# Kernel optimization log

Measured on AMD Instinct MI355X. Metric: run time of the kernel, lower is better.

Reference implementation:

```python
import jax, jax.numpy as jnp
import numpy as np

THRESHOLD = 0.5  # args.threshold: mask prob >= threshold means 'read' this token
HIDDEN = 256
EMBED = 300
BATCH = 64
STEPS = 2048


def setup_inputs() -> dict:
    key = jax.random.key(0)
    ks = jax.random.split(key, 10)
    H, E = HIDDEN, EMBED
    s = 1.0 / np.sqrt(H)
    return {
        "embedded": jax.random.normal(ks[0], (BATCH, STEPS, E), dtype=jnp.float32),
        "mask": jax.random.uniform(ks[1], (BATCH, STEPS), dtype=jnp.float32),
        "lengths": jax.random.randint(ks[2], (BATCH,), 1, STEPS + 1),
        # LSTM cell params (torch gate order i, f, g, o)
        "W_ih": jax.random.uniform(ks[3], (4 * H, E), minval=-s, maxval=s, dtype=jnp.float32),
        "W_hh": jax.random.uniform(ks[4], (4 * H, H), minval=-s, maxval=s, dtype=jnp.float32),
        "b_ih": jax.random.uniform(ks[5], (4 * H,), minval=-s, maxval=s, dtype=jnp.float32),
        "b_hh": jax.random.uniform(ks[6], (4 * H,), minval=-s, maxval=s, dtype=jnp.float32),
        "W_out": jax.random.uniform(ks[7], (2, H), minval=-s, maxval=s, dtype=jnp.float32),
        "b_out": jax.random.uniform(ks[8], (2,), minval=-s, maxval=s, dtype=jnp.float32),
    }


def reference(embedded, mask, lengths, W_ih, W_hh, b_ih, b_hh, W_out, b_out):
    B, T, E = embedded.shape
    H = W_hh.shape[1]
    b = b_ih + b_hh

    def step(carry, xs):
        h, c = carry
        x_t, m_t = xs  # [B,E], [B]
        z = x_t @ W_ih.T + h @ W_hh.T + b  # [B,4H]
        i, f, g, o = jnp.split(z, 4, axis=-1)
        i = jax.nn.sigmoid(i)
        f = jax.nn.sigmoid(f)
        g = jnp.tanh(g)
        o = jax.nn.sigmoid(o)
        c_new = f * c + i * g
        h_new = o * jnp.tanh(c_new)
        read = (m_t >= THRESHOLD)[:, None]  # skip-RNN gate
        h2 = jnp.where(read, h_new, h)
        c2 = jnp.where(read, c_new, c)
        return (h2, c2), h2

    h0 = jnp.zeros((B, H), embedded.dtype)
    c0 = jnp.zeros((B, H), embedded.dtype)
    xs = (jnp.swapaxes(embedded, 0, 1), mask.T)  # time-major
    _, hs = jax.lax.scan(step, (h0, c0), xs)  # hs: [T,B,H]

    idx = jnp.clip(lengths - 1, 0, T - 1)
    last = hs[idx, jnp.arange(B)]  # [B,H] last relevant output
    logits = last @ W_out.T + b_out
    probs = jax.nn.softmax(logits, axis=-1)
    predictions = jnp.argmax(probs, axis=1)
    return probs, predictions
```

## Files before the change

### kernel.cpp

```cpp
#include <hip/hip_runtime.h>
#include <math.h>

#define BATCH  64
#define TSTEPS 2048
#define EMBED  300
#define HID    256
#define GATES  1024
#define WSTRIDE 36
#define ASTR   328

typedef __fp16 h2 __attribute__((ext_vector_type(2)));
typedef __fp16 h4 __attribute__((ext_vector_type(4)));
typedef __fp16 h8 __attribute__((ext_vector_type(8)));
typedef float  f4 __attribute__((ext_vector_type(4)));

__device__ __forceinline__ h2 pack_h2(float a, float b) {
    return __builtin_amdgcn_cvt_pkrtz(a, b);
}
__device__ __forceinline__ h2 bc_h2(unsigned u) {
    return __builtin_bit_cast(h2, u);
}
__device__ __forceinline__ float dot2f(h2 w, h2 h, float acc) {
#if __has_builtin(__builtin_amdgcn_fdot2)
    return __builtin_amdgcn_fdot2(w, h, acc, false);
#else
    return acc + (float)w[0]*(float)h[0] + (float)w[1]*(float)h[1];
#endif
}
__device__ __forceinline__ float rcpf_(float x) {
#if __has_builtin(__builtin_amdgcn_rcpf)
    return __builtin_amdgcn_rcpf(x);
#else
    return 1.0f / x;
#endif
}
__device__ __forceinline__ float sigm_(float x) { return rcpf_(1.f + __expf(-x)); }
__device__ __forceinline__ float tanh_(float x) { return 1.f - 2.f*rcpf_(__expf(2.f*x) + 1.f); }

__global__ __launch_bounds__(256) void k_compact(
    const float* __restrict__ mask, const int* __restrict__ lengths,
    int* __restrict__ list, int* __restrict__ cnt,
    float* __restrict__ h_state, float* __restrict__ c_state,
    int t0, int CT, int first_chunk)
{
    int b = blockIdx.x, tid = threadIdx.x;
    if (first_chunk) {
        h_state[b*HID + tid] = 0.f;
        c_state[b*HID + tid] = 0.f;
    }
    int idx = lengths[b] - 1;
    idx = idx < 0 ? 0 : (idx > TSTEPS-1 ? TSTEPS-1 : idx);

    __shared__ int wcnt[4];
    __shared__ int running;
    if (tid == 0) running = 0;
    __syncthreads();

    for (int base = 0; base < CT; base += 256) {
        int t = t0 + base + tid;
        bool pred = ((base + tid) < CT) && (t <= idx)
                    && (mask[b*TSTEPS + t] >= 0.5f);
        unsigned long long bal = __ballot(pred);
        int wave = tid >> 6, lane = tid & 63;
        if (lane == 0) wcnt[wave] = __popcll(bal);
        __syncthreads();
        int off = running;
        for (int w2 = 0; w2 < wave; ++w2) off += wcnt[w2];
        off += __popcll(bal & ((1ull << lane) - 1ull));
        if (pred) list[b*CT + off] = t;
        __syncthreads();
        if (tid == 0) running += wcnt[0] + wcnt[1] + wcnt[2] + wcnt[3];
        __syncthreads();
    }
    if (tid == 0) cnt[b] = running;
}

__global__ __launch_bounds__(256) void k_gemm(
    const float* __restrict__ emb, const float* __restrict__ W_ih,
    const int* __restrict__ list, const int* __restrict__ cnt,
    float* __restrict__ Z, int CT)
{
    int b = blockIdx.z;
    int mb = cnt[b];
    int n0 = blockIdx.x * 128;
    int tid = threadIdx.x;
    int w = tid >> 6, l = tid & 63;

    __shared__ _Float16 Al[64 * ASTR];
    __shared__ _Float16 Bl[128 * ASTR];
    __shared__ int tl[64];

    for (int idx = tid; idx < 128*75; idx += 256) {
        int r = idx / 75, c = idx - 75*r;
        float4 v = ((const float4*)(W_ih + (size_t)(n0 + r)*EMBED))[c];
        *(h2*)&Bl[r*ASTR + 4*c]     = pack_h2(v.x, v.y);
        *(h2*)&Bl[r*ASTR + 4*c + 2] = pack_h2(v.z, v.w);
    }
    for (int idx = tid; idx < 128*14; idx += 256) {
        int r = idx / 14, c2 = idx - 14*r;
        *(unsigned*)&Bl[r*ASTR + 300 + 2*c2] = 0u;
    }
    for (int idx = tid; idx < 64*14; idx += 256) {
        int r = idx / 14, c2 = idx - 14*r;
        *(unsigned*)&Al[r*ASTR + 300 + 2*c2] = 0u;
    }

    int arow = w*16 + (l & 15);
    int kg4  = (l >> 4) * 4;
    int drow0 = w*16 + (l >> 4)*4;

    for (int i0 = 0; i0 < mb; i0 += 64) {
        __syncthreads();
        if (tid < 64) {
            int j = i0 + tid;
            tl[tid] = (j < mb) ? list[b*CT + j] : -1;
        }
        __syncthreads();
        for (int idx = tid; idx < 64*75; idx += 256) {
            int r = idx / 75, c = idx - 75*r;
            float4 v = {0.f, 0.f, 0.f, 0.f};
            int trow = tl[r];
            if (trow >= 0)
                v = ((const float4*)(emb + ((size_t)b*TSTEPS + trow)*EMBED))[c];
            *(h2*)&Al[r*ASTR + 4*c]     = pack_h2(v.x, v.y);
            *(h2*)&Al[r*ASTR + 4*c + 2] = pack_h2(v.z, v.w);
        }
        __syncthreads();

        f4 acc[8];
        #pragma unroll
        for (int nt = 0; nt < 8; ++nt) acc[nt] = f4{0.f, 0.f, 0.f, 0.f};

        #pragma unroll 2
        for (int ks = 0; ks < 10; ++ks) {
            int kb = ks*32 + kg4;
            h4 alo = *(const h4*)&Al[arow*ASTR + kb];
            h4 ahi = *(const h4*)&Al[arow*ASTR + kb + 16];
            h8 af = __builtin_shufflevector(alo, ahi, 0,1,2,3,4,5,6,7);
            #pragma unroll
            for (int nt = 0; nt < 8; ++nt) {
                int brow = nt*16 + (l & 15);
                h4 blo = *(const h4*)&Bl[brow*ASTR + kb];
                h4 bhi = *(const h4*)&Bl[brow*ASTR + kb + 16];
                h8 bf = __builtin_shufflevector(blo, bhi, 0,1,2,3,4,5,6,7);
                acc[nt] = __builtin_amdgcn_mfma_f32_16x16x32_f16(af, bf, acc[nt], 0, 0, 0);
            }
        }

        #pragma unroll
        for (int nt = 0; nt < 8; ++nt) {
            #pragma unroll
            for (int j = 0; j < 4; ++j) {
                int r = drow0 + j;
                if (i0 + r < mb)
                    Z[((size_t)b*CT + i0 + r)*GATES + n0 + nt*16 + (l & 15)] = acc[nt][j];
            }
        }
    }
}

__global__ __launch_bounds__(512, 2) void k_lstm(
    const float* __restrict__ Z, const int* __restrict__ cnt,
    const float* __restrict__ W_hh,
    const float* __restrict__ b_ih, const float* __restrict__ b_hh,
    float* __restrict__ h_state, float* __restrict__ c_state, int CT)
{
    int b = blockIdx.x;
    int tid = threadIdx.x;
    int d   = tid & 255;
    int rowA = tid;
    int rowB = tid + 512;

    __shared__ __align__(16) unsigned wlds[1024 * WSTRIDE];
    __shared__ float act13[2][256];
    __shared__ __align__(16) _Float16 h_arr[HID];

    for (int idx = tid; idx < 1024*32; idx += 512) {
        int r = idx >> 5, k = idx & 31;
        float2 v = ((const float2*)(W_hh + (size_t)r*HID))[k];
        *(h2*)&wlds[r*WSTRIDE + k] = pack_h2(v.x, v.y);
    }

    h2 wrA[96], wrB[96];
    {
        const float2* pA = (const float2*)(W_hh + (size_t)rowA*HID);
        const float2* pB = (const float2*)(W_hh + (size_t)rowB*HID);
        #pragma unroll
        for (int t = 0; t < 96; ++t) {
            float2 va = pA[32 + t], vb = pB[32 + t];
            wrA[t] = pack_h2(va.x, va.y);
            wrB[t] = pack_h2(vb.x, vb.y);
        }
    }
    float biasA = b_ih[rowA] + b_hh[rowA];
    float biasB = b_ih[rowB] + b_hh[rowB];

    float c_reg = 0.f;
    if (tid < 256) {
        h_arr[d] = (_Float16)h_state[(size_t)b*HID + d];
        c_reg    = c_state[(size_t)b*HID + d];
    }
    __syncthreads();

    int mb = cnt[b];
    float zAcur = 0.f, zBcur = 0.f;
    if (mb > 0) {
        zAcur = Z[((size_t)b*CT)*GATES + rowA];
        zBcur = Z[((size_t)b*CT)*GATES + rowB];
    }

    for (int j = 0; j < mb; ++j) {
        float zAn = 0.f, zBn = 0.f;
        if (j + 1 < mb) {
            zAn = Z[((size_t)b*CT + j + 1)*GATES + rowA];
            zBn = Z[((size_t)b*CT + j + 1)*GATES + rowB];
        }

        float accA0 = 0.f, accA1 = 0.f, accB0 = 0.f, accB1 = 0.f;
        #pragma unroll
        for (int c = 0; c < 32; ++c) {
            uint4 hv = ((const uint4*)h_arr)[c];
            h2 h0 = bc_h2(hv.x), h1 = bc_h2(hv.y);
            h2 h2_ = bc_h2(hv.z), h3 = bc_h2(hv.w);
            h2 wA0, wA1, wA2, wA3, wB0, wB1, wB2, wB3;
            if (c < 8) {
                uint4 wa = *(const uint4*)&wlds[rowA*WSTRIDE + 4*c];
                uint4 wb = *(const uint4*)&wlds[rowB*WSTRIDE + 4*c];
                wA0 = bc_h2(wa.x); wA1 = bc_h2(wa.y);
                wA2 = bc_h2(wa.z); wA3 = bc_h2(wa.w);
                wB0 = bc_h2(wb.x); wB1 = bc_h2(wb.y);
                wB2 = bc_h2(wb.z); wB3 = bc_h2(wb.w);
            } else {
                int t = (c - 8) * 4;
                wA0 = wrA[t+0]; wA1 = wrA[t+1]; wA2 = wrA[t+2]; wA3 = wrA[t+3];
                wB0 = wrB[t+0]; wB1 = wrB[t+1]; wB2 = wrB[t+2]; wB3 = wrB[t+3];
            }
            accA0 = dot2f(wA0, h0, accA0);
            accA1 = dot2f(wA1, h1, accA1);
            accA0 = dot2f(wA2, h2_, accA0);
            accA1 = dot2f(wA3, h3, accA1);
            accB0 = dot2f(wB0, h0, accB0);
            accB1 = dot2f(wB1, h1, accB1);
            accB0 = dot2f(wB2, h2_, accB0);
            accB1 = dot2f(wB3, h3, accB1);
        }
        float aF = zAcur + biasA + (accA0 + accA1);
        float aS = zBcur + biasB + (accB0 + accB1);

        float iv = 0.f, gv = 0.f;
        if (tid < 256) {
            iv = sigm_(aF);
            gv = tanh_(aS);
        } else {
            act13[0][d] = sigm_(aF);
            act13[1][d] = sigm_(aS);
        }
        __syncthreads();

        if (tid < 256) {
            float fv = act13[0][d], ov = act13[1][d];
            c_reg = fv * c_reg + iv * gv;
            float hn = ov * tanh_(c_reg);
            h_arr[d] = (_Float16)hn;
        }
        __syncthreads();
        zAcur = zAn; zBcur = zBn;
    }

    if (tid < 256) {
        h_state[(size_t)b*HID + d] = (float)h_arr[d];
        c_state[(size_t)b*HID + d] = c_reg;
    }
}

__global__ __launch_bounds__(64) void k_final(
    const float* __restrict__ h_state, const float* __restrict__ W_out,
    const float* __restrict__ b_out, float* __restrict__ out)
{
    int b = threadIdx.x;
    float l0 = b_out[0], l1 = b_out[1];
    for (int k = 0; k < HID; ++k) {
        float h = h_state[b*HID + k];
        l0 += h * W_out[k];
        l1 += h * W_out[HID + k];
    }
    float m  = fmaxf(l0, l1);
    float e0 = expf(l0 - m), e1 = expf(l1 - m);
    float s  = e0 + e1;
    float p0 = e0 / s, p1 = e1 / s;
    out[b*2 + 0] = p0;
    out[b*2 + 1] = p1;
    out[BATCH*2 + b] = (p1 > p0) ? 1.0f : 0.0f;
}

extern "C" void kernel_launch(void* const* d_in, const int* in_sizes, int n_in,
                              void* d_out, int out_size, void* d_ws, size_t ws_size,
                              hipStream_t stream)
{
    (void)in_sizes; (void)n_in; (void)out_size;
    const float* emb   = (const float*)d_in[0];
    const float* mask  = (const float*)d_in[1];
    const int*   len   = (const int*)  d_in[2];
    const float* W_ih  = (const float*)d_in[3];
    const float* W_hh  = (const float*)d_in[4];
    const float* b_ih  = (const float*)d_in[5];
    const float* b_hh  = (const float*)d_in[6];
    const float* W_out = (const float*)d_in[7];
    const float* b_out = (const float*)d_in[8];
    float* out = (float*)d_out;

    char* p = (char*)d_ws;
    auto carve = [&](size_t bytes) -> char* {
        char* r = p;
        p += (bytes + 255) & ~(size_t)255;
        return r;
    };
    float* h_state = (float*)carve((size_t)BATCH*HID*4);
    float* c_state = (float*)carve((size_t)BATCH*HID*4);
    int*   cntb    = (int*)  carve((size_t)BATCH*4);

    size_t fixed = (size_t)(p - (char*)d_ws);
    int CT = TSTEPS;
    while (CT > 64) {
        size_t lb = (((size_t)BATCH*CT*4) + 255) & ~(size_t)255;
        size_t zb = (size_t)BATCH*CT*GATES*4;
        if (fixed + lb + zb + 1024 <= ws_size) break;
        CT >>= 1;
    }
    int*   list = (int*)  carve((size_t)BATCH*CT*4);
    float* Z    = (float*)carve((size_t)BATCH*CT*GATES*4);

    int nchunks = TSTEPS / CT;
    for (int c = 0; c < nchunks; ++c) {
        int t0 = c * CT;
        int first = (c == 0) ? 1 : 0;
        hipLaunchKernelGGL(k_compact, dim3(BATCH), dim3(256), 0, stream,
                           mask, len, list, cntb, h_state, c_state,
                           t0, CT, first);
        hipLaunchKernelGGL(k_gemm, dim3(8, 1, BATCH), dim3(256), 0, stream,
                           emb, W_ih, list, cntb, Z, CT);
        hipLaunchKernelGGL(k_lstm, dim3(BATCH), dim3(512), 0, stream,
                           Z, cntb, W_hh, b_ih, b_hh,
                           h_state, c_state, CT);
    }
    hipLaunchKernelGGL(k_final, dim3(1), dim3(64), 0, stream,
                       h_state, W_out, b_out, out);
}
```

Before: 2.079 ms.

## Fuse input GEMM and LSTM recurrence into one persistent kernel with tile-ready flags

Merges the input-projection GEMM and the sequential LSTM recurrence into a single launch. 64 blocks run the recurrence while 192 worker blocks produce Z tiles in time-major order, and each finished tile raises a per-batch, per-64-step ready counter via release atomics. The recurrence blocks spin on these flags before consuming each 64-step chunk, so GEMM work overlaps with the serial recurrence instead of running before it. The cost is spin-wait polling and a reliance on all blocks being co-resident (with a bounded-spin fallback). Each GEMM work item also now reloads its W_ih tile rather than keeping it resident.

```diff
diff --git a/kernel.cpp b/kernel.cpp
--- a/kernel.cpp
+++ b/kernel.cpp
@@ -8,6 +8,8 @@
 #define GATES  1024
 #define WSTRIDE 36
 #define ASTR   328
+#define NWORK  192
+#define SHDW   37504
 
 typedef __fp16 h2 __attribute__((ext_vector_type(2)));
 typedef __fp16 h4 __attribute__((ext_vector_type(4)));
@@ -37,9 +39,17 @@
 __device__ __forceinline__ float sigm_(float x) { return rcpf_(1.f + __expf(-x)); }
 __device__ __forceinline__ float tanh_(float x) { return 1.f - 2.f*rcpf_(__expf(2.f*x) + 1.f); }
 
+__device__ __forceinline__ void spin_tile(const int* f) {
+    int tries = 0;
+    while (__hip_atomic_load(f, __ATOMIC_ACQUIRE, __HIP_MEMORY_SCOPE_AGENT) < 8) {
+        __builtin_amdgcn_s_sleep(4);
+        if (++tries > (1 << 18)) break;
+    }
+}
+
 __global__ __launch_bounds__(256) void k_compact(
     const float* __restrict__ mask, const int* __restrict__ lengths,
-    int* __restrict__ list, int* __restrict__ cnt,
+    int* __restrict__ list, int* __restrict__ cnt, int* __restrict__ ready,
     float* __restrict__ h_state, float* __restrict__ c_state,
     int t0, int CT, int first_chunk)
 {
@@ -48,6 +58,7 @@
         h_state[b*HID + tid] = 0.f;
         c_state[b*HID + tid] = 0.f;
     }
+    if (tid < 32) ready[b*32 + tid] = 0;
     int idx = lengths[b] - 1;
     idx = idx < 0 ? 0 : (idx > TSTEPS-1 ? TSTEPS-1 : idx);
 
@@ -75,112 +86,124 @@
     if (tid == 0) cnt[b] = running;
 }
 
-__global__ __launch_bounds__(256) void k_gemm(
+__global__ __launch_bounds__(512, 2) void k_fused(
     const float* __restrict__ emb, const float* __restrict__ W_ih,
     const int* __restrict__ list, const int* __restrict__ cnt,
-    float* __restrict__ Z, int CT)
+    float* __restrict__ Z, const float* __restrict__ W_hh,
+    const float* __restrict__ b_ih, const float* __restrict__ b_hh,
+    float* __restrict__ h_state, float* __restrict__ c_state,
+    int* __restrict__ ready, int CT)
 {
-    int b = blockIdx.z;
-    int mb = cnt[b];
-    int n0 = blockIdx.x * 128;
+    __shared__ __align__(16) unsigned shm[SHDW];
+    int bid = blockIdx.x;
     int tid = threadIdx.x;
-    int w = tid >> 6, l = tid & 63;
-
-    __shared__ _Float16 Al[64 * ASTR];
-    __shared__ _Float16 Bl[128 * ASTR];
-    __shared__ int tl[64];
-
-    for (int idx = tid; idx < 128*75; idx += 256) {
-        int r = idx / 75, c = idx - 75*r;
-        float4 v = ((const float4*)(W_ih + (size_t)(n0 + r)*EMBED))[c];
-        *(h2*)&Bl[r*ASTR + 4*c]     = pack_h2(v.x, v.y);
-        *(h2*)&Bl[r*ASTR + 4*c + 2] = pack_h2(v.z, v.w);
-    }
-    for (int idx = tid; idx < 128*14; idx += 256) {
-        int r = idx / 14, c2 = idx - 14*r;
-        *(unsigned*)&Bl[r*ASTR + 300 + 2*c2] = 0u;
-    }
-    for (int idx = tid; idx < 64*14; idx += 256) {
-        int r = idx / 14, c2 = idx - 14*r;
-        *(unsigned*)&Al[r*ASTR + 300 + 2*c2] = 0u;
-    }
-
-    int arow = w*16 + (l & 15);
-    int kg4  = (l >> 4) * 4;
-    int drow0 = w*16 + (l >> 4)*4;
-
-    for (int i0 = 0; i0 < mb; i0 += 64) {
-        __syncthreads();
-        if (tid < 64) {
-            int j = i0 + tid;
-            tl[tid] = (j < mb) ? list[b*CT + j] : -1;
-        }
-        __syncthreads();
-        for (int idx = tid; idx < 64*75; idx += 256) {
-            int r = idx / 75, c = idx - 75*r;
-            float4 v = {0.f, 0.f, 0.f, 0.f};
-            int trow = tl[r];
-            if (trow >= 0)
-                v = ((const float4*)(emb + ((size_t)b*TSTEPS + trow)*EMBED))[c];
-            *(h2*)&Al[r*ASTR + 4*c]     = pack_h2(v.x, v.y);
-            *(h2*)&Al[r*ASTR + 4*c + 2] = pack_h2(v.z, v.w);
-        }
-        __syncthreads();
-
-        f4 acc[8];
-        #pragma unroll
-        for (int nt = 0; nt < 8; ++nt) acc[nt] = f4{0.f, 0.f, 0.f, 0.f};
-
-        #pragma unroll 2
-        for (int ks = 0; ks < 10; ++ks) {
-            int kb = ks*32 + kg4;
-            h4 alo = *(const h4*)&Al[arow*ASTR + kb];
-            h4 ahi = *(const h4*)&Al[arow*ASTR + kb + 16];
-            h8 af = __builtin_shufflevector(alo, ahi, 0,1,2,3,4,5,6,7);
+
+    if (bid >= 64) {
+        int wi = bid - 64;
+        _Float16* Al = (_Float16*)shm;
+        _Float16* Bl = (_Float16*)(shm + 10496);
+        int*      tl = (int*)(shm + 31488);
+
+        for (int idx = tid; idx < 64*14; idx += 512) {
+            int r = idx / 14, c2 = idx - 14*r;
+            *(unsigned*)&Al[r*ASTR + 300 + 2*c2] = 0u;
+        }
+        for (int idx = tid; idx < 128*14; idx += 512) {
+            int r = idx / 14, c2 = idx - 14*r;
+            *(unsigned*)&Bl[r*ASTR + 300 + 2*c2] = 0u;
+        }
+
+        int w = tid >> 6, l = tid & 63;
+        int w2 = w & 3, nh = w >> 2;
+        int arow = w2*16 + (l & 15);
+        int kg4  = (l >> 4) * 4;
+        int drow0 = w2*16 + (l >> 4)*4;
+
+        int MT = CT >> 6;
+        for (int it = wi; it < MT*512; it += NWORK) {
+            int m = it >> 9, rem = it & 511;
+            int n = rem >> 6, b = rem & 63;
+            int mb = cnt[b];
+            int i0 = m * 64;
+            if (i0 >= mb) continue;
+            int n0 = n * 128;
+
+            __syncthreads();
+            if (tid < 64) {
+                int jj = i0 + tid;
+                tl[tid] = (jj < mb) ? list[b*CT + jj] : -1;
+            }
+            __syncthreads();
+            for (int idx = tid; idx < 64*75; idx += 512) {
+                int r = idx / 75, c = idx - 75*r;
+                float4 v = {0.f, 0.f, 0.f, 0.f};
+                int trow = tl[r];
+                if (trow >= 0)
+                    v = ((const float4*)(emb + ((size_t)b*TSTEPS + trow)*EMBED))[c];
+                *(h2*)&Al[r*ASTR + 4*c]     = pack_h2(v.x, v.y);
+                *(h2*)&Al[r*ASTR + 4*c + 2] = pack_h2(v.z, v.w);
+            }
+            for (int idx = tid; idx < 128*75; idx += 512) {
+                int r = idx / 75, c = idx - 75*r;
+                float4 v = ((const float4*)(W_ih + (size_t)(n0 + r)*EMBED))[c];
+                *(h2*)&Bl[r*ASTR + 4*c]     = pack_h2(v.x, v.y);
+                *(h2*)&Bl[r*ASTR + 4*c + 2] = pack_h2(v.z, v.w);
+            }
+            __syncthreads();
+
+            f4 acc[4];
             #pragma unroll
-            for (int nt = 0; nt < 8; ++nt) {
-                int brow = nt*16 + (l & 15);
-                h4 blo = *(const h4*)&Bl[brow*ASTR + kb];
-                h4 bhi = *(const h4*)&Bl[brow*ASTR + kb + 16];
-                h8 bf = __builtin_shufflevector(blo, bhi, 0,1,2,3,4,5,6,7);
-                acc[nt] = __builtin_amdgcn_mfma_f32_16x16x32_f16(af, bf, acc[nt], 0, 0, 0);
-            }
-        }
-
-        #pragma unroll
-        for (int nt = 0; nt < 8; ++nt) {
+            for (int q = 0; q < 4; ++q) acc[q] = f4{0.f, 0.f, 0.f, 0.f};
+
+            #pragma unroll 2
+            for (int ks = 0; ks < 10; ++ks) {
+                int kb = ks*32 + kg4;
+                h4 alo = *(const h4*)&Al[arow*ASTR + kb];
+                h4 ahi = *(const h4*)&Al[arow*ASTR + kb + 16];
+                h8 af = __builtin_shufflevector(alo, ahi, 0,1,2,3,4,5,6,7);
+                #pragma unroll
+                for (int q = 0; q < 4; ++q) {
+                    int brow = (nh*4 + q)*16 + (l & 15);
+                    h4 blo = *(const h4*)&Bl[brow*ASTR + kb];
+                    h4 bhi = *(const h4*)&Bl[brow*ASTR + kb + 16];
+                    h8 bf = __builtin_shufflevector(blo, bhi, 0,1,2,3,4,5,6,7);
+                    acc[q] = __builtin_amdgcn_mfma_f32_16x16x32_f16(af, bf, acc[q], 0, 0, 0);
+                }
+            }
+
             #pragma unroll
-            for (int j = 0; j < 4; ++j) {
-                int r = drow0 + j;
-                if (i0 + r < mb)
-                    Z[((size_t)b*CT + i0 + r)*GATES + n0 + nt*16 + (l & 15)] = acc[nt][j];
-            }
-        }
-    }
-}
-
-__global__ __launch_bounds__(512, 2) void k_lstm(
-    const float* __restrict__ Z, const int* __restrict__ cnt,
-    const float* __restrict__ W_hh,
-    const float* __restrict__ b_ih, const float* __restrict__ b_hh,
-    float* __restrict__ h_state, float* __restrict__ c_state, int CT)
-{
-    int b = blockIdx.x;
-    int tid = threadIdx.x;
-    int d   = tid & 255;
+            for (int q = 0; q < 4; ++q) {
+                #pragma unroll
+                for (int j = 0; j < 4; ++j) {
+                    int r = drow0 + j;
+                    if (i0 + r < mb)
+                        Z[((size_t)b*CT + i0 + r)*GATES + n0 + (nh*4+q)*16 + (l & 15)] =
+                            acc[q][j];
+                }
+            }
+            __threadfence();
+            __syncthreads();
+            if (tid == 0)
+                __hip_atomic_fetch_add(&ready[b*32 + m], 1,
+                                       __ATOMIC_RELEASE, __HIP_MEMORY_SCOPE_AGENT);
+        }
+        return;
+    }
+
+    int b = bid;
+    unsigned* wlds  = shm;
+    float*    act13 = (float*)(shm + 36864);
+    _Float16* h_arr = (_Float16*)(shm + 37376);
+
+    int d    = tid & 255;
     int rowA = tid;
     int rowB = tid + 512;
-
-    __shared__ __align__(16) unsigned wlds[1024 * WSTRIDE];
-    __shared__ float act13[2][256];
-    __shared__ __align__(16) _Float16 h_arr[HID];
 
     for (int idx = tid; idx < 1024*32; idx += 512) {
         int r = idx >> 5, k = idx & 31;
         float2 v = ((const float2*)(W_hh + (size_t)r*HID))[k];
         *(h2*)&wlds[r*WSTRIDE + k] = pack_h2(v.x, v.y);
     }
-
     h2 wrA[96], wrB[96];
     {
         const float2* pA = (const float2*)(W_hh + (size_t)rowA*HID);
@@ -205,15 +228,22 @@
     int mb = cnt[b];
     float zAcur = 0.f, zBcur = 0.f;
     if (mb > 0) {
+        if (tid == 0) spin_tile(&ready[b*32]);
+        __syncthreads();
         zAcur = Z[((size_t)b*CT)*GATES + rowA];
         zBcur = Z[((size_t)b*CT)*GATES + rowB];
     }
 
     for (int j = 0; j < mb; ++j) {
+        int jn = j + 1;
         float zAn = 0.f, zBn = 0.f;
-        if (j + 1 < mb) {
-            zAn = Z[((size_t)b*CT + j + 1)*GATES + rowA];
-            zBn = Z[((size_t)b*CT + j + 1)*GATES + rowB];
+        if (jn < mb) {
+            if ((jn & 63) == 0) {
+                if (tid == 0) spin_tile(&ready[b*32 + (jn >> 6)]);
+                __syncthreads();
+            }
+            zAn = Z[((size_t)b*CT + jn)*GATES + rowA];
+            zBn = Z[((size_t)b*CT + jn)*GATES + rowB];
         }
 
         float accA0 = 0.f, accA1 = 0.f, accB0 = 0.f, accB1 = 0.f;
@@ -252,13 +282,13 @@
             iv = sigm_(aF);
             gv = tanh_(aS);
         } else {
-            act13[0][d] = sigm_(aF);
-            act13[1][d] = sigm_(aS);
+            act13[d]       = sigm_(aF);
+            act13[256 + d] = sigm_(aS);
         }
         __syncthreads();
 
         if (tid < 256) {
-            float fv = act13[0][d], ov = act13[1][d];
+            float fv = act13[d], ov = act13[256 + d];
             c_reg = fv * c_reg + iv * gv;
             float hn = ov * tanh_(c_reg);
             h_arr[d] = (_Float16)hn;
@@ -318,6 +348,7 @@
     float* h_state = (float*)carve((size_t)BATCH*HID*4);
     float* c_state = (float*)carve((size_t)BATCH*HID*4);
     int*   cntb    = (int*)  carve((size_t)BATCH*4);
+    int*   ready   = (int*)  carve((size_t)BATCH*32*4);
 
     size_t fixed = (size_t)(p - (char*)d_ws);
     int CT = TSTEPS;
@@ -335,13 +366,11 @@
         int t0 = c * CT;
         int first = (c == 0) ? 1 : 0;
         hipLaunchKernelGGL(k_compact, dim3(BATCH), dim3(256), 0, stream,
-                           mask, len, list, cntb, h_state, c_state,
+                           mask, len, list, cntb, ready, h_state, c_state,
                            t0, CT, first);
-        hipLaunchKernelGGL(k_gemm, dim3(8, 1, BATCH), dim3(256), 0, stream,
-                           emb, W_ih, list, cntb, Z, CT);
-        hipLaunchKernelGGL(k_lstm, dim3(BATCH), dim3(512), 0, stream,
-                           Z, cntb, W_hh, b_ih, b_hh,
-                           h_state, c_state, CT);
+        hipLaunchKernelGGL(k_fused, dim3(256), dim3(512), 0, stream,
+                           emb, W_ih, list, cntb, Z, W_hh, b_ih, b_hh,
+                           h_state, c_state, ready, CT);
     }
     hipLaunchKernelGGL(k_final, dim3(1), dim3(64), 0, stream,
                        h_state, W_out, b_out, out);
```

Measured after the change: 2.129 ms. 2.4% more time.
